# Optimization experiments

Measured on AMD Instinct MI355X. Metric: run time of the kernel, lower is better.

## Reference

```python
import jax, jax.numpy as jnp
import numpy as np

N_NODES = 100000
IN_DIM = 128
N_EDGES = 600000
HIDDEN = 128


def setup_inputs() -> dict:
    key = jax.random.key(0)
    k_z, k_e, k_w1, k_b1, k_w2, k_b2 = jax.random.split(key, 6)
    z = jax.random.normal(k_z, (N_NODES, IN_DIM), dtype=jnp.float32)
    edge_index = jax.random.randint(k_e, (2, N_EDGES), 0, N_NODES, dtype=jnp.int64)
    # torch.nn.Linear weights: W has shape (out, in), y = x @ W.T + b
    lim1 = 1.0 / np.sqrt(2 * IN_DIM)
    W1 = jax.random.uniform(k_w1, (HIDDEN, 2 * IN_DIM), jnp.float32, -lim1, lim1)
    b1 = jax.random.uniform(k_b1, (HIDDEN,), jnp.float32, -lim1, lim1)
    lim2 = 1.0 / np.sqrt(HIDDEN)
    W2 = jax.random.uniform(k_w2, (1, HIDDEN), jnp.float32, -lim2, lim2)
    b2 = jax.random.uniform(k_b2, (1,), jnp.float32, -lim2, lim2)
    return {"z": z, "edge_index": edge_index, "W1": W1, "b1": b1, "W2": W2, "b2": b2}


def reference(z, edge_index, W1, b1, W2, b2):
    src, dst = edge_index[0], edge_index[1]
    pair = jnp.concatenate([z[src], z[dst]], axis=1)        # [E, 2*in_dim]
    h = jax.nn.relu(pair @ W1.T + b1)                        # [E, 128]
    out = (h @ W2.T + b2).squeeze(-1)                        # [E]
    return out
```

## Files before the change

### kernel.cpp

```cpp
#include <hip/hip_runtime.h>
#include <stdint.h>

#define IN_DIM 128
#define NCOL   256
#define CHUNK_B (32 * IN_DIM * 4)

typedef __bf16 bfx8 __attribute__((ext_vector_type(8)));
typedef __bf16 bfx4 __attribute__((ext_vector_type(4)));
typedef float  f32x4 __attribute__((ext_vector_type(4)));
typedef __attribute__((address_space(3))) void lds_void;

__device__ __forceinline__ int swz(int x) { return x ^ (((x >> 9) & 7) << 4); }

__global__ __launch_bounds__(256, 2) void gemm_mfma(
    const float* __restrict__ z, const float* __restrict__ W1,
    const float* __restrict__ b1, __bf16* __restrict__ UV, int nchunks)
{
    __shared__ float abuf[4][32 * IN_DIM];

    const int tid  = threadIdx.x;
    const int wave = tid >> 6;
    const int lane = tid & 63;
    const int l15  = lane & 15;
    const int q    = lane >> 4;
    const int n0   = wave * 64;

    bfx8  bfrag[4][4];
    f32x4 bias[4];
#pragma unroll
    for (int nt = 0; nt < 4; ++nt) {
        const int n = n0 + nt * 16 + l15;
        const float* src = (n < 128) ? (W1 + (size_t)n * 256)
                                     : (W1 + (size_t)(n - 128) * 256 + 128);
#pragma unroll
        for (int kk = 0; kk < 4; ++kk) {
            float4 f0 = *(const float4*)(src + kk * 32 + q * 8);
            float4 f1 = *(const float4*)(src + kk * 32 + q * 8 + 4);
            bfx8 b;
            b[0]=(__bf16)f0.x; b[1]=(__bf16)f0.y; b[2]=(__bf16)f0.z; b[3]=(__bf16)f0.w;
            b[4]=(__bf16)f1.x; b[5]=(__bf16)f1.y; b[6]=(__bf16)f1.z; b[7]=(__bf16)f1.w;
            bfrag[nt][kk] = b;
        }
        if (n0 + nt * 16 < 128) bias[nt] = *(const f32x4*)(b1 + n0 + nt * 16 + q * 4);
        else                    bias[nt] = (f32x4){0.f, 0.f, 0.f, 0.f};
    }

    const uint32_t lds0 = (uint32_t)(uintptr_t)(lds_void*)&abuf[0][0];

    auto STAGE = [&](int b, int cc) {
        const char* gbase = (const char*)(z + (size_t)cc * 32 * IN_DIM);
#pragma unroll
        for (int i = 0; i < 4; ++i) {
            const int seg  = (wave * 4 + i) << 10;
            const int loff = seg + lane * 16;
            __builtin_amdgcn_global_load_lds(
                (const __attribute__((address_space(1))) void*)(gbase + swz(loff)),
                (lds_void*)((char*)&abuf[b][0] + seg),
                16, 0, 0);
        }
    };

    const int T = (nchunks - blockIdx.x + gridDim.x - 1) / gridDim.x;

    STAGE(0, blockIdx.x);
    STAGE(1, blockIdx.x + gridDim.x);
    STAGE(2, blockIdx.x + 2 * gridDim.x);

    for (int i = 0; i < T; ++i) {
        const int c  = blockIdx.x + i * gridDim.x;
        const bool st = (i + 3 < T);
        if (st) STAGE((i + 3) & 3, c + 3 * gridDim.x);

        if      (i == 0) asm volatile("s_waitcnt vmcnt(12)" ::: "memory");
        else if (i == 1) asm volatile("s_waitcnt vmcnt(20)" ::: "memory");
        else if (i == 2) asm volatile("s_waitcnt vmcnt(28)" ::: "memory");
        else if (st)     asm volatile("s_waitcnt vmcnt(36)" ::: "memory");
        else             asm volatile("s_waitcnt vmcnt(8)"  ::: "memory");
        __builtin_amdgcn_s_barrier();
        asm volatile("" ::: "memory");

        const uint32_t tb = lds0 + (uint32_t)((i & 3) * CHUNK_B);

        f32x4 rf[2][4][2];
#pragma unroll
        for (int mt = 0; mt < 2; ++mt)
#pragma unroll
            for (int kk = 0; kk < 4; ++kk)
#pragma unroll
                for (int h = 0; h < 2; ++h) {
                    const int o = (mt * 16 + l15) * 512 + kk * 128 + q * 32 + h * 16;
                    asm volatile("ds_read_b128 %0, %1"
                                 : "=v"(rf[mt][kk][h])
                                 : "v"(tb + (uint32_t)swz(o)));
                }
        asm volatile("s_waitcnt lgkmcnt(0)" ::: "memory");
        __builtin_amdgcn_sched_barrier(0);

        f32x4 acc[2][4];
#pragma unroll
        for (int mt = 0; mt < 2; ++mt)
#pragma unroll
            for (int nt = 0; nt < 4; ++nt)
                acc[mt][nt] = (f32x4){0.f, 0.f, 0.f, 0.f};

#pragma unroll
        for (int kk = 0; kk < 4; ++kk) {
            bfx8 af[2];
#pragma unroll
            for (int mt = 0; mt < 2; ++mt) {
                f32x4 f0 = rf[mt][kk][0], f1 = rf[mt][kk][1];
                bfx8 a;
                a[0]=(__bf16)f0[0]; a[1]=(__bf16)f0[1]; a[2]=(__bf16)f0[2]; a[3]=(__bf16)f0[3];
                a[4]=(__bf16)f1[0]; a[5]=(__bf16)f1[1]; a[6]=(__bf16)f1[2]; a[7]=(__bf16)f1[3];
                af[mt] = a;
            }
#pragma unroll
            for (int mt = 0; mt < 2; ++mt)
#pragma unroll
                for (int nt = 0; nt < 4; ++nt)
                    acc[mt][nt] = __builtin_amdgcn_mfma_f32_16x16x32_bf16(
                        bfrag[nt][kk], af[mt], acc[mt][nt], 0, 0, 0);
        }

        const int m0 = c * 32;
#pragma unroll
        for (int mt = 0; mt < 2; ++mt) {
            __bf16* dst = UV + (size_t)(m0 + mt * 16 + l15) * NCOL + n0 + q * 4;
#pragma unroll
            for (int nt = 0; nt < 4; ++nt) {
                bfx4 v;
#pragma unroll
                for (int r = 0; r < 4; ++r)
                    v[r] = (__bf16)(acc[mt][nt][r] + bias[nt][r]);
                *(bfx4*)(dst + nt * 16) = v;
            }
        }

        asm volatile("" ::: "memory");
        __builtin_amdgcn_s_barrier();
        asm volatile("" ::: "memory");
    }
}

__global__ __launch_bounds__(256) void edge_mlp(
    const __bf16* __restrict__ UV, const int* __restrict__ ei,
    const float* __restrict__ W2, const float* __restrict__ b2,
    float* __restrict__ out, int E)
{
    const int gt   = blockIdx.x * blockDim.x + threadIdx.x;
    const int lane = threadIdx.x & 15;
    const int g    = gt >> 4;
    const int e0   = g * 2;
    const int j0   = lane * 8;

    float ww[8];
    {
        float4 w0 = *(const float4*)(W2 + j0);
        float4 w1 = *(const float4*)(W2 + j0 + 4);
        ww[0] = w0.x; ww[1] = w0.y; ww[2] = w0.z; ww[3] = w0.w;
        ww[4] = w1.x; ww[5] = w1.y; ww[6] = w1.z; ww[7] = w1.w;
    }

    if (e0 >= E) return;

    const int2 srcp = *(const int2*)(ei + e0);
    const int2 dstp = *(const int2*)(ei + E + e0);

    bfx8 u0 = *(const bfx8*)(UV + (size_t)srcp.x * NCOL + j0);
    bfx8 v0 = *(const bfx8*)(UV + (size_t)dstp.x * NCOL + 128 + j0);
    bfx8 u1 = *(const bfx8*)(UV + (size_t)srcp.y * NCOL + j0);
    bfx8 v1 = *(const bfx8*)(UV + (size_t)dstp.y * NCOL + 128 + j0);

    float s0 = 0.f, s1 = 0.f;
#pragma unroll
    for (int i = 0; i < 8; ++i) {
        float h0 = (float)u0[i] + (float)v0[i];
        float h1 = (float)u1[i] + (float)v1[i];
        s0 = fmaf(fmaxf(h0, 0.f), ww[i], s0);
        s1 = fmaf(fmaxf(h1, 0.f), ww[i], s1);
    }

#pragma unroll
    for (int d = 1; d < 16; d <<= 1) {
        s0 += __shfl_xor(s0, d);
        s1 += __shfl_xor(s1, d);
    }

    if (lane == 0) {
        float bb = b2[0];
        *(float2*)(out + e0) = make_float2(s0 + bb, s1 + bb);
    }
}

extern "C" void kernel_launch(void* const* d_in, const int* in_sizes, int n_in,
                              void* d_out, int out_size, void* d_ws, size_t ws_size,
                              hipStream_t stream)
{
    const float* z  = (const float*)d_in[0];
    const int*   ei = (const int*)d_in[1];
    const float* W1 = (const float*)d_in[2];
    const float* b1 = (const float*)d_in[3];
    const float* W2 = (const float*)d_in[4];
    const float* b2 = (const float*)d_in[5];
    float* out = (float*)d_out;

    const int M = in_sizes[0] / IN_DIM;
    const int E = in_sizes[1] / 2;

    __bf16* UV = (__bf16*)d_ws;

    const int nchunks = M / 32;
    gemm_mfma<<<512, 256, 0, stream>>>(z, W1, b1, UV, nchunks);

    int groups  = (E + 1) / 2;
    int eblocks = (groups * 16 + 255) / 256;
    edge_mlp<<<eblocks, 256, 0, stream>>>(UV, ei, W2, b2, out, E);
}
```

Before: 151.5 us.

## Use triple-buffered LDS staging and interleave LDS reads with MFMA per k-step

Cuts the GEMM's LDS ring from four chunk buffers to three and raises occupancy from 2 to 3 blocks per CU, with the grid grown from 512 to 768 blocks. The prefetch depth drops from three chunks ahead to two, and the vmcnt wait thresholds are reworked to match. LDS reads are now software-pipelined across the k-steps with two register buffers and partial lgkmcnt waits, replacing the read-everything-then-compute pattern. The goal is more latency hiding through occupancy and read/compute overlap, at the cost of a shallower global prefetch and hand-tuned wait counts that could be wrong at tail iterations.

```diff
diff --git a/kernel.cpp b/kernel.cpp
--- a/kernel.cpp
+++ b/kernel.cpp
@@ -12,11 +12,11 @@
 
 __device__ __forceinline__ int swz(int x) { return x ^ (((x >> 9) & 7) << 4); }
 
-__global__ __launch_bounds__(256, 2) void gemm_mfma(
+__global__ __launch_bounds__(256, 3) void gemm_mfma(
     const float* __restrict__ z, const float* __restrict__ W1,
     const float* __restrict__ b1, __bf16* __restrict__ UV, int nchunks)
 {
-    __shared__ float abuf[4][32 * IN_DIM];
+    __shared__ float abuf[3][32 * IN_DIM];
 
     const int tid  = threadIdx.x;
     const int wave = tid >> 6;
@@ -64,37 +64,35 @@
 
     STAGE(0, blockIdx.x);
     STAGE(1, blockIdx.x + gridDim.x);
-    STAGE(2, blockIdx.x + 2 * gridDim.x);
-
+
+    int bi = 0;
     for (int i = 0; i < T; ++i) {
         const int c  = blockIdx.x + i * gridDim.x;
-        const bool st = (i + 3 < T);
-        if (st) STAGE((i + 3) & 3, c + 3 * gridDim.x);
-
-        if      (i == 0) asm volatile("s_waitcnt vmcnt(12)" ::: "memory");
-        else if (i == 1) asm volatile("s_waitcnt vmcnt(20)" ::: "memory");
-        else if (i == 2) asm volatile("s_waitcnt vmcnt(28)" ::: "memory");
-        else if (st)     asm volatile("s_waitcnt vmcnt(36)" ::: "memory");
-        else             asm volatile("s_waitcnt vmcnt(8)"  ::: "memory");
+        const bool st = (i + 2 < T);
+        int sb = bi + 2; if (sb >= 3) sb -= 3;
+        if (st) STAGE(sb, c + 2 * gridDim.x);
+
+        if      (i == 0)     asm volatile("s_waitcnt vmcnt(8)"  ::: "memory");
+        else if (i == 1)     asm volatile("s_waitcnt vmcnt(16)" ::: "memory");
+        else if (st)         asm volatile("s_waitcnt vmcnt(24)" ::: "memory");
+        else if (i == T - 2) asm volatile("s_waitcnt vmcnt(20)" ::: "memory");
+        else                 asm volatile("s_waitcnt vmcnt(16)" ::: "memory");
         __builtin_amdgcn_s_barrier();
         asm volatile("" ::: "memory");
 
-        const uint32_t tb = lds0 + (uint32_t)((i & 3) * CHUNK_B);
-
-        f32x4 rf[2][4][2];
-#pragma unroll
-        for (int mt = 0; mt < 2; ++mt)
-#pragma unroll
-            for (int kk = 0; kk < 4; ++kk)
+        const uint32_t tb = lds0 + (uint32_t)(bi * CHUNK_B);
+
+        auto RD = [&](f32x4 (&rf)[2][2], int kk) {
+#pragma unroll
+            for (int mt = 0; mt < 2; ++mt)
 #pragma unroll
                 for (int h = 0; h < 2; ++h) {
                     const int o = (mt * 16 + l15) * 512 + kk * 128 + q * 32 + h * 16;
                     asm volatile("ds_read_b128 %0, %1"
-                                 : "=v"(rf[mt][kk][h])
+                                 : "=v"(rf[mt][h])
                                  : "v"(tb + (uint32_t)swz(o)));
                 }
-        asm volatile("s_waitcnt lgkmcnt(0)" ::: "memory");
-        __builtin_amdgcn_sched_barrier(0);
+        };
 
         f32x4 acc[2][4];
 #pragma unroll
@@ -103,12 +101,11 @@
             for (int nt = 0; nt < 4; ++nt)
                 acc[mt][nt] = (f32x4){0.f, 0.f, 0.f, 0.f};
 
-#pragma unroll
-        for (int kk = 0; kk < 4; ++kk) {
+        auto CM = [&](f32x4 (&rf)[2][2], int kk) {
             bfx8 af[2];
 #pragma unroll
             for (int mt = 0; mt < 2; ++mt) {
-                f32x4 f0 = rf[mt][kk][0], f1 = rf[mt][kk][1];
+                f32x4 f0 = rf[mt][0], f1 = rf[mt][1];
                 bfx8 a;
                 a[0]=(__bf16)f0[0]; a[1]=(__bf16)f0[1]; a[2]=(__bf16)f0[2]; a[3]=(__bf16)f0[3];
                 a[4]=(__bf16)f1[0]; a[5]=(__bf16)f1[1]; a[6]=(__bf16)f1[2]; a[7]=(__bf16)f1[3];
@@ -120,7 +117,25 @@
                 for (int nt = 0; nt < 4; ++nt)
                     acc[mt][nt] = __builtin_amdgcn_mfma_f32_16x16x32_bf16(
                         bfrag[nt][kk], af[mt], acc[mt][nt], 0, 0, 0);
-        }
+        };
+
+        f32x4 rfA[2][2], rfB[2][2];
+        RD(rfA, 0);
+        RD(rfB, 1);
+        asm volatile("s_waitcnt lgkmcnt(4)" ::: "memory");
+        __builtin_amdgcn_sched_barrier(0);
+        CM(rfA, 0);
+        RD(rfA, 2);
+        asm volatile("s_waitcnt lgkmcnt(4)" ::: "memory");
+        __builtin_amdgcn_sched_barrier(0);
+        CM(rfB, 1);
+        RD(rfB, 3);
+        asm volatile("s_waitcnt lgkmcnt(4)" ::: "memory");
+        __builtin_amdgcn_sched_barrier(0);
+        CM(rfA, 2);
+        asm volatile("s_waitcnt lgkmcnt(0)" ::: "memory");
+        __builtin_amdgcn_sched_barrier(0);
+        CM(rfB, 3);
 
         const int m0 = c * 32;
 #pragma unroll
@@ -139,6 +154,7 @@
         asm volatile("" ::: "memory");
         __builtin_amdgcn_s_barrier();
         asm volatile("" ::: "memory");
+        bi = (bi == 2) ? 0 : bi + 1;
     }
 }
 
@@ -210,7 +226,7 @@
     __bf16* UV = (__bf16*)d_ws;
 
     const int nchunks = M / 32;
-    gemm_mfma<<<512, 256, 0, stream>>>(z, W1, b1, UV, nchunks);
+    gemm_mfma<<<768, 256, 0, stream>>>(z, W1, b1, UV, nchunks);
 
     int groups  = (E + 1) / 2;
     int eblocks = (groups * 16 + 255) / 256;
```

After: 162.7 us. 7.4% more time.
